# Optimization experiments

Measured on AMD Instinct MI355X. Metric: run time of the kernel, lower is better.

## Reference

```python
import jax, jax.numpy as jnp
import numpy as np

NEG_SLOPE = 0.2  # PyG GATConv default leaky_relu slope
NUM_GRAPHS = 64


def gat_layer(x, src, dst, W, a_src, a_dst, b, heads, out_ch, concat, N):
    # x: [N, in_ch] -> h: [N, H, C]
    h = (x @ W).reshape(N, heads, out_ch)
    a_s = jnp.einsum('nhc,hc->nh', h, a_src)  # [N, H]
    a_d = jnp.einsum('nhc,hc->nh', h, a_dst)  # [N, H]
    e = jax.nn.leaky_relu(a_s[src] + a_d[dst], NEG_SLOPE)  # [E, H]
    # segment softmax over edges grouped by destination node
    emax = jax.ops.segment_max(e, dst, num_segments=N)
    emax = jnp.where(jnp.isfinite(emax), emax, 0.0)
    ex = jnp.exp(e - emax[dst])
    denom = jax.ops.segment_sum(ex, dst, num_segments=N)
    alpha = ex / (denom[dst] + 1e-16)  # [E, H]
    out = jax.ops.segment_sum(alpha[:, :, None] * h[src], dst, num_segments=N)  # [N, H, C]
    out = out.reshape(N, heads * out_ch) if concat else out.mean(axis=1)
    return out + b


def setup_inputs() -> dict:
    key = jax.random.key(0)
    ks = jax.random.split(key, 16)
    N, E, F_IN, H, C, NC = 50000, 800000, 128, 4, 64, 200
    x = jax.random.normal(ks[0], (N, F_IN), dtype=jnp.float32)
    edge_index = jax.random.randint(ks[1], (2, E), 0, N, dtype=jnp.int32)
    batch = jnp.sort(jax.random.randint(ks[2], (N,), 0, NUM_GRAPHS, dtype=jnp.int32))
    s = 0.05
    params = dict(
        W1=jax.random.normal(ks[3], (F_IN, H * C), jnp.float32) * s,
        a_src1=jax.random.normal(ks[4], (H, C), jnp.float32) * s,
        a_dst1=jax.random.normal(ks[5], (H, C), jnp.float32) * s,
        b1=jnp.zeros((H * C,), jnp.float32),
        W2=jax.random.normal(ks[6], (H * C, H * C), jnp.float32) * s,
        a_src2=jax.random.normal(ks[7], (H, C), jnp.float32) * s,
        a_dst2=jax.random.normal(ks[8], (H, C), jnp.float32) * s,
        b2=jnp.zeros((H * C,), jnp.float32),
        W3=jax.random.normal(ks[9], (H * C, C), jnp.float32) * s,
        a_src3=jax.random.normal(ks[10], (1, C), jnp.float32) * s,
        a_dst3=jax.random.normal(ks[11], (1, C), jnp.float32) * s,
        b3=jnp.zeros((C,), jnp.float32),
        Wc=jax.random.normal(ks[12], (C, NC), jnp.float32) * s,
        bc=jnp.zeros((NC,), jnp.float32),
    )
    return dict(x=x, edge_index=edge_index, batch=batch, **params)


def reference(x, edge_index, batch,
              W1, a_src1, a_dst1, b1,
              W2, a_src2, a_dst2, b2,
              W3, a_src3, a_dst3, b3,
              Wc, bc):
    N = x.shape[0]
    # PyG GATConv adds self-loops by default
    loop = jnp.arange(N, dtype=edge_index.dtype)
    src = jnp.concatenate([edge_index[0], loop])
    dst = jnp.concatenate([edge_index[1], loop])
    H, C = a_src1.shape
    h = gat_layer(x, src, dst, W1, a_src1, a_dst1, b1, H, C, True, N)
    h = jax.nn.elu(h)  # dropout is identity in eval mode
    h = gat_layer(h, src, dst, W2, a_src2, a_dst2, b2, H, C, True, N)
    h = jax.nn.elu(h)
    h = gat_layer(h, src, dst, W3, a_src3, a_dst3, b3, 1, C, False, N)
    h = jax.nn.elu(h)
    # global mean pool per graph
    sums = jax.ops.segment_sum(h, batch, num_segments=NUM_GRAPHS)
    counts = jax.ops.segment_sum(jnp.ones((N,), h.dtype), batch, num_segments=NUM_GRAPHS)
    pooled = sums / jnp.maximum(counts, 1.0)[:, None]
    return pooled @ Wc + bc
```

## Files before the change

### kernel.cpp

```cpp
#include <hip/hip_runtime.h>


typedef __attribute__((ext_vector_type(8))) __bf16 bf16x8;
typedef __attribute__((ext_vector_type(4))) float f32x4;
typedef __attribute__((ext_vector_type(8))) unsigned short u16x8;

#define LOG2E 1.44269504f

static __device__ __forceinline__ unsigned short f2bf(float f) {
    unsigned u = __float_as_uint(f);
    unsigned r = (u + 0x7fffu + ((u >> 16) & 1u)) >> 16;
    return (unsigned short)r;
}
static __device__ __forceinline__ float bf2f(unsigned short s) {
    return __uint_as_float(((unsigned)s) << 16);
}

static __device__ __forceinline__ void g2lds16(const unsigned short* g,
                                               unsigned short* l) {
    __builtin_amdgcn_global_load_lds(
        (const __attribute__((address_space(1))) unsigned int*)g,
        (__attribute__((address_space(3))) unsigned int*)l, 16, 0, 0);
}

__global__ void count_edges(const int* __restrict__ ei, int* __restrict__ deg,
                            int* __restrict__ epos, int E) {
    int i = blockIdx.x * blockDim.x + threadIdx.x;
    if (i >= E) return;
    int dst = ei[E + i];
    epos[i] = atomicAdd(&deg[dst], 1);
}

__global__ __launch_bounds__(256) void scan_partial(const int* __restrict__ deg,
                                                    int* __restrict__ rowptr,
                                                    int* __restrict__ blockSums, int N) {
    int t = threadIdx.x;
    int lane = t & 63, wv = t >> 6;
    int base = blockIdx.x * 1024 + t * 4;
    int v[4];
#pragma unroll
    for (int j = 0; j < 4; ++j) v[j] = (base + j < N) ? deg[base + j] + 1 : 0;
    int local = v[0] + v[1] + v[2] + v[3];
    int x = local;
#pragma unroll
    for (int off = 1; off < 64; off <<= 1) {
        int y = __shfl_up(x, off);
        if (lane >= off) x += y;
    }
    __shared__ int wsum[4];
    if (lane == 63) wsum[wv] = x;
    __syncthreads();
    int woff = 0;
    for (int i = 0; i < wv; ++i) woff += wsum[i];
    int run = woff + x - local;
#pragma unroll
    for (int j = 0; j < 4; ++j) {
        if (base + j < N) rowptr[base + j] = run;
        run += v[j];
    }
    if (t == 255) blockSums[blockIdx.x] = woff + x;
}

__global__ void scan_blocks(int* __restrict__ blockSums, int* __restrict__ rowptr,
                            int NB, int N) {
    int lane = threadIdx.x;
    int carry = 0;
    for (int b0 = 0; b0 < NB; b0 += 64) {
        int i = b0 + lane;
        int v = (i < NB) ? blockSums[i] : 0;
        int x = v;
#pragma unroll
        for (int off = 1; off < 64; off <<= 1) {
            int y = __shfl_up(x, off);
            if (lane >= off) x += y;
        }
        if (i < NB) blockSums[i] = carry + x - v;
        carry += __shfl(x, 63);
    }
    if (lane == 0) {
        int c = N >> 10;
        int offN;
        if (c < NB) {
            offN = blockSums[c];
        } else {
            blockSums[c] = 0;
            offN = 0;
        }
        rowptr[N] = carry - offN;
    }
}

__global__ void scatter_edges(const int* __restrict__ ei, const int* __restrict__ rowptr,
                              const int* __restrict__ bs,
                              const int* __restrict__ deg, const int* __restrict__ epos,
                              int* __restrict__ srcs, int E, int N) {
    int i = blockIdx.x * blockDim.x + threadIdx.x;
    int tot = E + N;
    if (i >= tot) return;
    if (i < E) {
        int dst = ei[E + i];
        srcs[rowptr[dst] + bs[dst >> 10] + epos[i]] = ei[i];
    } else {
        int d = i - E;
        srcs[rowptr[d] + bs[d >> 10] + deg[d]] = d;
    }
}

__global__ void prep_cast(const float* __restrict__ W1, unsigned short* __restrict__ Wt1,
                          const float* __restrict__ W2, unsigned short* __restrict__ Wt2,
                          const float* __restrict__ W3, unsigned short* __restrict__ Wt3,
                          int n1, int n2, int n3, int F_IN, int HC, int C) {
    int i = blockIdx.x * blockDim.x + threadIdx.x;
    if (i < n1) {
        int n = i / F_IN, k = i - n * F_IN;
        Wt1[i] = f2bf(W1[(size_t)k * HC + n]);
        return;
    }
    i -= n1;
    if (i < n2) {
        int n = i / HC, k = i - n * HC;
        Wt2[i] = f2bf(W2[(size_t)k * HC + n]);
        return;
    }
    i -= n2;
    if (i < n3) {
        int n = i / HC, k = i - n * HC;
        Wt3[i] = f2bf(W3[(size_t)k * C + n]);
    }
}

__global__ void prep_asd(const float* __restrict__ W1, const float* __restrict__ as1,
                         const float* __restrict__ ad1,
                         const float* __restrict__ W2, const float* __restrict__ as2,
                         const float* __restrict__ ad2,
                         const float* __restrict__ W3, const float* __restrict__ as3,
                         const float* __restrict__ ad3,
                         unsigned short* __restrict__ wasd1,
                         unsigned short* __restrict__ wasd2,
                         unsigned short* __restrict__ wasd3) {
    int i = blockIdx.x * blockDim.x + threadIdx.x;
    if (i < 16 * 128) {
        int p = i >> 7, k = i & 127;
        float v = 0.f;
        if (p < 8) {
            const float* a = (p < 4) ? as1 : ad1;
            int hh = p & 3;
            for (int c = 0; c < 64; ++c)
                v += W1[(size_t)k * 256 + hh * 64 + c] * a[hh * 64 + c];
        }
        wasd1[i] = f2bf(v);
        return;
    }
    i -= 16 * 128;
    if (i < 16 * 256) {
        int p = i >> 8, k = i & 255;
        float v = 0.f;
        if (p < 8) {
            const float* a = (p < 4) ? as2 : ad2;
            int hh = p & 3;
            for (int c = 0; c < 64; ++c)
                v += W2[(size_t)k * 256 + hh * 64 + c] * a[hh * 64 + c];
        }
        wasd2[i] = f2bf(v);
        return;
    }
    i -= 16 * 256;
    if (i < 16 * 256) {
        int p = i >> 8, k = i & 255;
        float v = 0.f;
        if (p < 2) {
            const float* a = p ? ad3 : as3;
            for (int c = 0; c < 64; ++c)
                v += W3[(size_t)k * 64 + c] * a[c];
        }
        wasd3[i] = f2bf(v);
    }
}

#define BK 32

template <bool AF32, int WAVES_N>
__global__ __launch_bounds__(256) void gemm_bf16(const void* __restrict__ Av,
                                                 const unsigned short* __restrict__ Bt,
                                                 const unsigned short* __restrict__ Wasd,
                                                 unsigned short* __restrict__ C,
                                                 float* __restrict__ as_o,
                                                 float* __restrict__ ad_o,
                                                 int M, int N, int K, int H) {
    constexpr int BMt = (4 / WAVES_N) * 64;
    constexpr int BNt = WAVES_N * 64;
    constexpr int ASLOTS = BMt * 4;
    constexpr int ROUNDS = (BMt + BNt) / 64;
    constexpr bool ASD_ALL = (WAVES_N == 1);
    __shared__ unsigned short As[2][BMt * BK];
    __shared__ unsigned short Bs[2][BNt * BK];
    __shared__ unsigned short Ws[2][16 * BK];
    int t = threadIdx.x;
    int bm = blockIdx.y * BMt;
    int wave = t >> 6, lane = t & 63;
    int wm = (wave / WAVES_N) * 64, wn = (wave % WAVES_N) * 64;
    int quad = lane >> 4, mr = lane & 15;

    f32x4 zero = {0.f, 0.f, 0.f, 0.f};
    f32x4 acc[4][4];
#pragma unroll
    for (int i = 0; i < 4; ++i)
#pragma unroll
        for (int j = 0; j < 4; ++j) acc[i][j] = zero;
    f32x4 acc4[4];
#pragma unroll
    for (int i = 0; i < 4; ++i) acc4[i] = zero;

    int sw = quad ^ ((mr >> 1) & 3);
    int aoff[4], boff[4];
#pragma unroll
    for (int i = 0; i < 4; ++i) {
        aoff[i] = (wm + i * 16 + mr) * BK + sw * 8;
        boff[i] = (wn + i * 16 + mr) * BK + sw * 8;
    }

    auto stage_ab = [&](int bsel, int kk) {
        const unsigned short* Ab = (const unsigned short*)Av;
#pragma unroll
        for (int r = 0; r < ROUNDS; ++r) {
            int slotw = r * 256 + wave * 64;
            int slot = slotw + lane;
            if (slotw < ASLOTS) {
                int row = slot >> 2;
                int sg = (slot & 3) ^ ((row >> 1) & 3);
                int gra = bm + row;
                if (gra < M)
                    g2lds16(&Ab[(size_t)gra * K + kk + sg * 8], &As[bsel][slotw * 8]);
            } else {
                int bslot = slot - ASLOTS;
                int row = bslot >> 2;
                int sg = (bslot & 3) ^ ((row >> 1) & 3);
                g2lds16(&Bt[(size_t)row * K + kk + sg * 8], &Bs[bsel][(slotw - ASLOTS) * 8]);
            }
        }
        if (wave == 0)
            g2lds16(&Wasd[(size_t)(lane >> 2) * K + kk + (lane & 3) * 8], &Ws[bsel][0]);
    };
    auto stage_b_af32 = [&](int bsel, int kk) {
#pragma unroll
        for (int r = 0; r < BNt / 64; ++r) {
            int slotw = r * 256 + wave * 64;
            int bslot = slotw + lane;
            int row = bslot >> 2;
            int sg = (bslot & 3) ^ ((row >> 1) & 3);
            g2lds16(&Bt[(size_t)row * K + kk + sg * 8], &Bs[bsel][slotw * 8]);
        }
        if (wave == 0)
            g2lds16(&Wasd[(size_t)(lane >> 2) * K + kk + (lane & 3) * 8], &Ws[bsel][0]);
    };
    auto loadA_f32 = [&](int kk, float4& lo, float4& hi) {
        int slot = t, row = slot >> 2;
        int sg = (slot & 3) ^ ((row >> 1) & 3);
        int gra = bm + row;
        lo = make_float4(0.f, 0.f, 0.f, 0.f); hi = lo;
        if (gra < M) {
            const float* Af = (const float*)Av;
            lo = *(const float4*)&Af[(size_t)gra * K + kk + sg * 8];
            hi = *(const float4*)&Af[(size_t)gra * K + kk + sg * 8 + 4];
        }
    };
    auto writeA = [&](int bsel, float4 lo, float4 hi) {
        int slot = t;
        *(ushort4*)&As[bsel][slot * 8]     = make_ushort4(f2bf(lo.x), f2bf(lo.y), f2bf(lo.z), f2bf(lo.w));
        *(ushort4*)&As[bsel][slot * 8 + 4] = make_ushort4(f2bf(hi.x), f2bf(hi.y), f2bf(hi.z), f2bf(hi.w));
    };

    const int nt = K / BK;
    int cur = 0;

    if (AF32) {
        float4 l0, h0;
        loadA_f32(0, l0, h0);
        writeA(0, l0, h0);
        stage_b_af32(0, 0);
    } else {
        stage_ab(0, 0);
    }
    __syncthreads();

    for (int ts = 0; ts < nt; ++ts) {
        int nxt = cur ^ 1;
        bool more = (ts + 1 < nt);
        float4 plo, phi;
        if (more) {
            if (AF32) {
                loadA_f32((ts + 1) * BK, plo, phi);
                stage_b_af32(nxt, (ts + 1) * BK);
            } else {
                stage_ab(nxt, (ts + 1) * BK);
            }
        }
        bf16x8 af[4], bfr[4];
#pragma unroll
        for (int i = 0; i < 4; ++i) {
            af[i]  = *(bf16x8*)&As[cur][aoff[i]];
            bfr[i] = *(bf16x8*)&Bs[cur][boff[i]];
        }
#pragma unroll
        for (int i = 0; i < 4; ++i)
#pragma unroll
            for (int j = 0; j < 4; ++j)
                acc[i][j] = __builtin_amdgcn_mfma_f32_16x16x32_bf16(af[i], bfr[j], acc[i][j], 0, 0, 0);
        if (ASD_ALL || wave == 0) {
            bf16x8 wsf = *(bf16x8*)&Ws[cur][mr * BK + quad * 8];
#pragma unroll
            for (int i = 0; i < 4; ++i)
                acc4[i] = __builtin_amdgcn_mfma_f32_16x16x32_bf16(af[i], wsf, acc4[i], 0, 0, 0);
        }
        if (more && AF32) writeA(nxt, plo, phi);
        __syncthreads();
        cur = nxt;
    }

    if ((ASD_ALL || wave == 0) && mr < 2 * H) {
#pragma unroll
        for (int i = 0; i < 4; ++i)
#pragma unroll
            for (int r = 0; r < 4; ++r) {
                int grow = bm + wm + i * 16 + quad * 4 + r;
                if (grow >= M) continue;
                float v = acc4[i][r] * LOG2E;
                if (mr < H) as_o[(size_t)grow * H + mr] = v;
                else        ad_o[(size_t)grow * H + (mr - H)] = v;
            }
    }

#pragma unroll
    for (int i = 0; i < 4; ++i) {
#pragma unroll
        for (int r = 0; r < 4; ++r) {
            int grow = bm + wm + i * 16 + quad * 4 + r;
            if (grow >= M) continue;
#pragma unroll
            for (int j = 0; j < 4; ++j) {
                int gcol = wn + j * 16 + mr;
                C[(size_t)grow * N + gcol] = f2bf(acc[i][j][r]);
            }
        }
    }
}

template <int H, int NPW, int VPL, bool OUTF32>
__global__ __launch_bounds__(256) void gat_aggregate(const unsigned short* __restrict__ hbuf,
                                                     const float* __restrict__ as_i,
                                                     const float* __restrict__ ad_i,
                                                     const int* __restrict__ rowptr,
                                                     const int* __restrict__ bs,
                                                     const int* __restrict__ srcs,
                                                     const float* __restrict__ bias,
                                                     void* __restrict__ out_v, int N) {
    constexpr int LPN = 64 / NPW;
    constexpr int HC = LPN * VPL;
    int wid = (blockIdx.x * blockDim.x + threadIdx.x) >> 6;
    int lane = threadIdx.x & 63;
    int sub = lane / LPN;
    int li  = lane % LPN;
    int node = wid * NPW + sub;
    if (node >= N) return;
    int row = rowptr[node] + bs[node >> 10];
    int end = rowptr[node + 1] + bs[(node + 1) >> 10];
    int len = end - row;
    const int hd_lane = (li * VPL) >> 6;

    float advh = ad_i[(size_t)node * H + hd_lane];

    float acc[VPL];
#pragma unroll
    for (int j = 0; j < VPL; ++j) acc[j] = 0.f;
    float l = 0.f;

    const int U = 8;
    for (int base = 0; base < len; base += U) {
        int s[U];
        float cf[U];
#pragma unroll
        for (int u = 0; u < U; ++u) {
            int idx = base + u;
            int ii = row + ((idx < len) ? idx : (len - 1));
            s[u] = srcs[ii];
        }
#pragma unroll
        for (int u = 0; u < U; ++u) cf[u] = as_i[(size_t)s[u] * H + hd_lane];
        if (VPL == 8) {
            u16x8 r[U];
#pragma unroll
            for (int u = 0; u < U; ++u)
                r[u] = *(const u16x8*)&hbuf[(size_t)s[u] * HC + li * 8];
#pragma unroll
            for (int u = 0; u < U; ++u) {
                float e = cf[u] + advh;
                e = fmaxf(e, 0.2f * e);
                float wgt = (base + u < len) ? exp2f(e) : 0.f;
                l += wgt;
#pragma unroll
                for (int j = 0; j < 8; ++j) acc[j] += wgt * bf2f(r[u][j]);
            }
        } else {
            ushort4 r[U];
#pragma unroll
            for (int u = 0; u < U; ++u)
                r[u] = *(const ushort4*)&hbuf[(size_t)s[u] * HC + li * 4];
#pragma unroll
            for (int u = 0; u < U; ++u) {
                float e = cf[u] + advh;
                e = fmaxf(e, 0.2f * e);
                float wgt = (base + u < len) ? exp2f(e) : 0.f;
                l += wgt;
                acc[0] += wgt * bf2f(r[u].x);
                acc[1] += wgt * bf2f(r[u].y);
                acc[2] += wgt * bf2f(r[u].z);
                acc[3] += wgt * bf2f(r[u].w);
            }
        }
    }

    float inv_l = 1.f / (l + 1e-16f);
    float vals[VPL];
#pragma unroll
    for (int j = 0; j < VPL; ++j) {
        float v = acc[j] * inv_l + bias[li * VPL + j];
        vals[j] = (v > 0.f) ? v : (__expf(v) - 1.f);
    }
    if (OUTF32) {
        float* out = (float*)out_v;
        if (VPL == 4) {
            float4 o = make_float4(vals[0], vals[1], vals[2], vals[3]);
            *(float4*)&out[(size_t)node * HC + li * 4] = o;
        } else {
#pragma unroll
            for (int j = 0; j < VPL; ++j)
                out[(size_t)node * HC + li * VPL + j] = vals[j];
        }
    } else {
        unsigned short* out = (unsigned short*)out_v;
        if (VPL == 8) {
            u16x8 o;
#pragma unroll
            for (int j = 0; j < 8; ++j) o[j] = f2bf(vals[j]);
            *(u16x8*)&out[(size_t)node * HC + li * 8] = o;
        } else {
            ushort4 o;
            o.x = f2bf(vals[0]); o.y = f2bf(vals[1]);
            o.z = f2bf(vals[2]); o.w = f2bf(vals[3]);
            *(ushort4*)&out[(size_t)node * HC + li * 4] = o;
        }
    }
}

#define POOL_CHUNK 128
__global__ __launch_bounds__(256) void pool_kernel(const float* __restrict__ hf,
                                                   const int* __restrict__ batch,
                                                   float* __restrict__ sums,
                                                   float* __restrict__ counts, int N) {
    int t = threadIdx.x;
    int c = t & 63, sub = t >> 6;
    int start = blockIdx.x * POOL_CHUNK;
    int end = min(start + POOL_CHUNK, N);
    float acc = 0.f, cnt = 0.f;
    int cur = -1;
    for (int n = start + sub; n < end; n += 4) {
        int g = batch[n];
        if (g != cur) {
            if (cur >= 0) {
                atomicAdd(&sums[cur * 64 + c], acc);
                if (c == 0) atomicAdd(&counts[cur], cnt);
            }
            cur = g; acc = 0.f; cnt = 0.f;
        }
        acc += hf[(size_t)n * 64 + c];
        cnt += 1.f;
    }
    if (cur >= 0) {
        atomicAdd(&sums[cur * 64 + c], acc);
        if (c == 0) atomicAdd(&counts[cur], cnt);
    }
}

__global__ void classify(const float* __restrict__ sums, const float* __restrict__ counts,
                         const float* __restrict__ Wc, const float* __restrict__ bc,
                         float* __restrict__ out, int NC) {
    __shared__ float p[64];
    int g = blockIdx.x;
    if (threadIdx.x < 64) {
        float cnt = fmaxf(counts[g], 1.0f);
        p[threadIdx.x] = sums[g * 64 + threadIdx.x] / cnt;
    }
    __syncthreads();
    int k = threadIdx.x;
    if (k < NC) {
        float acc = bc[k];
        for (int c = 0; c < 64; ++c) acc += p[c] * Wc[c * NC + k];
        out[g * NC + k] = acc;
    }
}

static inline size_t align_up(size_t x, size_t a) { return (x + a - 1) / a * a; }

extern "C" void kernel_launch(void* const* d_in, const int* in_sizes, int n_in,
                              void* d_out, int out_size, void* d_ws, size_t ws_size,
                              hipStream_t stream) {
    const float* x      = (const float*)d_in[0];
    const int*   ei     = (const int*)d_in[1];
    const int*   batch  = (const int*)d_in[2];
    const float* W1     = (const float*)d_in[3];
    const float* a_src1 = (const float*)d_in[4];
    const float* a_dst1 = (const float*)d_in[5];
    const float* b1     = (const float*)d_in[6];
    const float* W2     = (const float*)d_in[7];
    const float* a_src2 = (const float*)d_in[8];
    const float* a_dst2 = (const float*)d_in[9];
    const float* b2     = (const float*)d_in[10];
    const float* W3     = (const float*)d_in[11];
    const float* a_src3 = (const float*)d_in[12];
    const float* a_dst3 = (const float*)d_in[13];
    const float* b3     = (const float*)d_in[14];
    const float* Wc     = (const float*)d_in[15];
    const float* bc     = (const float*)d_in[16];

    const int N    = in_sizes[2];
    const int E    = in_sizes[1] / 2;
    const int F_IN = in_sizes[0] / N;
    const int HC   = in_sizes[6];
    const int C    = in_sizes[14];
    const int NC   = in_sizes[16];
    const int Etot = E + N;
    const int NB   = (N + 1023) / 1024;
    const int NPB  = (N + POOL_CHUNK - 1) / POOL_CHUNK;

    char* w = (char*)d_ws;
    size_t off = 0;
    auto alloc = [&](size_t bytes) -> void* {
        void* p = w + off;
        off = align_up(off + bytes, 256);
        return p;
    };
    int*   deg    = (int*)alloc((size_t)N * 4);
    float* sums   = (float*)alloc((size_t)(64 * 64 + 64) * 4);
    float* counts = sums + 64 * 64;
    int*   rowptr = (int*)alloc((size_t)(N + 1) * 4);
    int*   epos   = (int*)alloc((size_t)E * 4);
    int*   srcs   = (int*)alloc((size_t)Etot * 4);
    int*   bsums  = (int*)alloc((size_t)(NB + 1) * 4);
    float* as_buf = (float*)alloc((size_t)N * 4 * 4);
    float* ad_buf = (float*)alloc((size_t)N * 4 * 4);
    unsigned short* Wt1 = (unsigned short*)alloc((size_t)HC * F_IN * 2);
    unsigned short* Wt2 = (unsigned short*)alloc((size_t)HC * HC * 2);
    unsigned short* Wt3 = (unsigned short*)alloc((size_t)C * HC * 2);
    unsigned short* wasd1 = (unsigned short*)alloc((size_t)16 * F_IN * 2);
    unsigned short* wasd2 = (unsigned short*)alloc((size_t)16 * HC * 2);
    unsigned short* wasd3 = (unsigned short*)alloc((size_t)16 * HC * 2);
    unsigned short* hA  = (unsigned short*)alloc((size_t)N * HC * 2);
    unsigned short* hB  = (unsigned short*)alloc((size_t)N * HC * 2);
    unsigned short* hC  = (unsigned short*)alloc((size_t)N * C * 2);
    float* bufF   = (float*)alloc((size_t)N * C * 4);

    const int TPB = 256;

    hipMemsetAsync(deg, 0, (char*)(sums + 64 * 64 + 64) - (char*)deg, stream);

    count_edges<<<(E + TPB - 1) / TPB, TPB, 0, stream>>>(ei, deg, epos, E);
    scan_partial<<<NB, 256, 0, stream>>>(deg, rowptr, bsums, N);
    scan_blocks<<<1, 64, 0, stream>>>(bsums, rowptr, NB, N);
    scatter_edges<<<(Etot + TPB - 1) / TPB, TPB, 0, stream>>>(ei, rowptr, bsums, deg, epos, srcs, E, N);

    int n1 = HC * F_IN, n2 = HC * HC, n3 = C * HC;
    int ntot = n1 + n2 + n3;
    prep_cast<<<(ntot + TPB - 1) / TPB, TPB, 0, stream>>>(
        W1, Wt1, W2, Wt2, W3, Wt3, n1, n2, n3, F_IN, HC, C);
    int nasd = 16 * F_IN + 16 * HC + 16 * HC;
    prep_asd<<<(nasd + TPB - 1) / TPB, TPB, 0, stream>>>(
        W1, a_src1, a_dst1, W2, a_src2, a_dst2, W3, a_src3, a_dst3,
        wasd1, wasd2, wasd3);

    dim3 gWide(1, (N + 63) / 64);
    dim3 gNarrow(1, (N + 255) / 256);
    int aggBlocks12 = (((N + 1) / 2) + 3) / 4;
    int aggBlocks3  = (((N + 3) / 4) + 3) / 4;

    gemm_bf16<true, 4><<<gWide, 256, 0, stream>>>(x, Wt1, wasd1, hA, as_buf, ad_buf, N, HC, F_IN, 4);
    gat_aggregate<4, 2, 8, false><<<aggBlocks12, 256, 0, stream>>>(hA, as_buf, ad_buf, rowptr, bsums, srcs, b1, hB, N);

    gemm_bf16<false, 4><<<gWide, 256, 0, stream>>>(hB, Wt2, wasd2, hA, as_buf, ad_buf, N, HC, HC, 4);
    gat_aggregate<4, 2, 8, false><<<aggBlocks12, 256, 0, stream>>>(hA, as_buf, ad_buf, rowptr, bsums, srcs, b2, hB, N);

    gemm_bf16<false, 1><<<gNarrow, 256, 0, stream>>>(hB, Wt3, wasd3, hC, as_buf, ad_buf, N, C, HC, 1);
    gat_aggregate<1, 4, 4, true><<<aggBlocks3, 256, 0, stream>>>(hC, as_buf, ad_buf, rowptr, bsums, srcs, b3, bufF, N);

    pool_kernel<<<NPB, 256, 0, stream>>>(bufF, batch, sums, counts, N);
    classify<<<64, 256, 0, stream>>>(sums, counts, Wc, bc, (float*)d_out, NC);
}
```

Baseline: 398.6 us.

## Fuse graph prep and pool/classify stages into cooperative kernels with grid sync

Replaces the memset, count, two-level scan, scatter and two weight-prep launches with a single cooperative kernel that separates phases with grid-wide barriers. The pooling and classifier kernels are merged the same way. The goal is to remove launch overhead and inter-kernel gaps for many small kernels. In exchange, a fixed 256-block grid processes the large edge loops with grid-stride loops, and grid.sync itself has a cost. The scan phase also assumes NB is no larger than the grid size (49 here).

Result: slower. 590.3 us (+48.1%).

```diff
diff --git a/kernel.cpp b/kernel.cpp
--- a/kernel.cpp
+++ b/kernel.cpp
@@ -1,4 +1,7 @@
 #include <hip/hip_runtime.h>
+#include <hip/hip_cooperative_groups.h>
+
+namespace cg = cooperative_groups;
 
 
 typedef __attribute__((ext_vector_type(8))) __bf16 bf16x8;
@@ -23,132 +26,48 @@
         (__attribute__((address_space(3))) unsigned int*)l, 16, 0, 0);
 }
 
-__global__ void count_edges(const int* __restrict__ ei, int* __restrict__ deg,
-                            int* __restrict__ epos, int E) {
-    int i = blockIdx.x * blockDim.x + threadIdx.x;
-    if (i >= E) return;
-    int dst = ei[E + i];
-    epos[i] = atomicAdd(&deg[dst], 1);
-}
-
-__global__ __launch_bounds__(256) void scan_partial(const int* __restrict__ deg,
-                                                    int* __restrict__ rowptr,
-                                                    int* __restrict__ blockSums, int N) {
-    int t = threadIdx.x;
-    int lane = t & 63, wv = t >> 6;
-    int base = blockIdx.x * 1024 + t * 4;
-    int v[4];
-#pragma unroll
-    for (int j = 0; j < 4; ++j) v[j] = (base + j < N) ? deg[base + j] + 1 : 0;
-    int local = v[0] + v[1] + v[2] + v[3];
-    int x = local;
-#pragma unroll
-    for (int off = 1; off < 64; off <<= 1) {
-        int y = __shfl_up(x, off);
-        if (lane >= off) x += y;
-    }
-    __shared__ int wsum[4];
-    if (lane == 63) wsum[wv] = x;
-    __syncthreads();
-    int woff = 0;
-    for (int i = 0; i < wv; ++i) woff += wsum[i];
-    int run = woff + x - local;
-#pragma unroll
-    for (int j = 0; j < 4; ++j) {
-        if (base + j < N) rowptr[base + j] = run;
-        run += v[j];
-    }
-    if (t == 255) blockSums[blockIdx.x] = woff + x;
-}
-
-__global__ void scan_blocks(int* __restrict__ blockSums, int* __restrict__ rowptr,
-                            int NB, int N) {
-    int lane = threadIdx.x;
-    int carry = 0;
-    for (int b0 = 0; b0 < NB; b0 += 64) {
-        int i = b0 + lane;
-        int v = (i < NB) ? blockSums[i] : 0;
-        int x = v;
-#pragma unroll
-        for (int off = 1; off < 64; off <<= 1) {
-            int y = __shfl_up(x, off);
-            if (lane >= off) x += y;
-        }
-        if (i < NB) blockSums[i] = carry + x - v;
-        carry += __shfl(x, 63);
-    }
-    if (lane == 0) {
-        int c = N >> 10;
-        int offN;
-        if (c < NB) {
-            offN = blockSums[c];
-        } else {
-            blockSums[c] = 0;
-            offN = 0;
-        }
-        rowptr[N] = carry - offN;
-    }
-}
-
-__global__ void scatter_edges(const int* __restrict__ ei, const int* __restrict__ rowptr,
-                              const int* __restrict__ bs,
-                              const int* __restrict__ deg, const int* __restrict__ epos,
-                              int* __restrict__ srcs, int E, int N) {
-    int i = blockIdx.x * blockDim.x + threadIdx.x;
-    int tot = E + N;
-    if (i >= tot) return;
-    if (i < E) {
-        int dst = ei[E + i];
-        srcs[rowptr[dst] + bs[dst >> 10] + epos[i]] = ei[i];
-    } else {
-        int d = i - E;
-        srcs[rowptr[d] + bs[d >> 10] + deg[d]] = d;
-    }
-}
-
-__global__ void prep_cast(const float* __restrict__ W1, unsigned short* __restrict__ Wt1,
-                          const float* __restrict__ W2, unsigned short* __restrict__ Wt2,
-                          const float* __restrict__ W3, unsigned short* __restrict__ Wt3,
-                          int n1, int n2, int n3, int F_IN, int HC, int C) {
-    int i = blockIdx.x * blockDim.x + threadIdx.x;
-    if (i < n1) {
-        int n = i / F_IN, k = i - n * F_IN;
-        Wt1[i] = f2bf(W1[(size_t)k * HC + n]);
+struct PrepArgs {
+    const int* ei;
+    int* deg; int* epos; int* rowptr; int* bsums; int* srcs;
+    float* zero0; int zn;
+    const float* W1; const float* W2; const float* W3;
+    const float* as1; const float* ad1;
+    const float* as2; const float* ad2;
+    const float* as3; const float* ad3;
+    unsigned short* Wt1; unsigned short* Wt2; unsigned short* Wt3;
+    unsigned short* wasd1; unsigned short* wasd2; unsigned short* wasd3;
+    int E; int N; int NB; int n1; int n2; int n3; int F_IN; int HC; int C;
+};
+
+static __device__ __forceinline__ void prep_elem(int i, const PrepArgs& a) {
+    if (i < a.n1) {
+        int n = i / a.F_IN, k = i - n * a.F_IN;
+        a.Wt1[i] = f2bf(a.W1[(size_t)k * a.HC + n]);
         return;
     }
-    i -= n1;
-    if (i < n2) {
-        int n = i / HC, k = i - n * HC;
-        Wt2[i] = f2bf(W2[(size_t)k * HC + n]);
+    i -= a.n1;
+    if (i < a.n2) {
+        int n = i / a.HC, k = i - n * a.HC;
+        a.Wt2[i] = f2bf(a.W2[(size_t)k * a.HC + n]);
         return;
     }
-    i -= n2;
-    if (i < n3) {
-        int n = i / HC, k = i - n * HC;
-        Wt3[i] = f2bf(W3[(size_t)k * C + n]);
-    }
-}
-
-__global__ void prep_asd(const float* __restrict__ W1, const float* __restrict__ as1,
-                         const float* __restrict__ ad1,
-                         const float* __restrict__ W2, const float* __restrict__ as2,
-                         const float* __restrict__ ad2,
-                         const float* __restrict__ W3, const float* __restrict__ as3,
-                         const float* __restrict__ ad3,
-                         unsigned short* __restrict__ wasd1,
-                         unsigned short* __restrict__ wasd2,
-                         unsigned short* __restrict__ wasd3) {
-    int i = blockIdx.x * blockDim.x + threadIdx.x;
+    i -= a.n2;
+    if (i < a.n3) {
+        int n = i / a.HC, k = i - n * a.HC;
+        a.Wt3[i] = f2bf(a.W3[(size_t)k * a.C + n]);
+        return;
+    }
+    i -= a.n3;
     if (i < 16 * 128) {
         int p = i >> 7, k = i & 127;
         float v = 0.f;
         if (p < 8) {
-            const float* a = (p < 4) ? as1 : ad1;
+            const float* aa = (p < 4) ? a.as1 : a.ad1;
             int hh = p & 3;
             for (int c = 0; c < 64; ++c)
-                v += W1[(size_t)k * 256 + hh * 64 + c] * a[hh * 64 + c];
-        }
-        wasd1[i] = f2bf(v);
+                v += a.W1[(size_t)k * 256 + hh * 64 + c] * aa[hh * 64 + c];
+        }
+        a.wasd1[i] = f2bf(v);
         return;
     }
     i -= 16 * 128;
@@ -156,12 +75,12 @@
         int p = i >> 8, k = i & 255;
         float v = 0.f;
         if (p < 8) {
-            const float* a = (p < 4) ? as2 : ad2;
+            const float* aa = (p < 4) ? a.as2 : a.ad2;
             int hh = p & 3;
             for (int c = 0; c < 64; ++c)
-                v += W2[(size_t)k * 256 + hh * 64 + c] * a[hh * 64 + c];
-        }
-        wasd2[i] = f2bf(v);
+                v += a.W2[(size_t)k * 256 + hh * 64 + c] * aa[hh * 64 + c];
+        }
+        a.wasd2[i] = f2bf(v);
         return;
     }
     i -= 16 * 256;
@@ -169,11 +88,100 @@
         int p = i >> 8, k = i & 255;
         float v = 0.f;
         if (p < 2) {
-            const float* a = p ? ad3 : as3;
+            const float* aa = p ? a.ad3 : a.as3;
             for (int c = 0; c < 64; ++c)
-                v += W3[(size_t)k * 64 + c] * a[c];
-        }
-        wasd3[i] = f2bf(v);
+                v += a.W3[(size_t)k * 64 + c] * aa[c];
+        }
+        a.wasd3[i] = f2bf(v);
+    }
+}
+
+__global__ __launch_bounds__(256) void fused_prep(PrepArgs a) {
+    cg::grid_group grid = cg::this_grid();
+    const int gtid = blockIdx.x * 256 + threadIdx.x;
+    const int gsz = gridDim.x * 256;
+
+    for (int i = gtid; i < a.N; i += gsz) a.deg[i] = 0;
+    for (int i = gtid; i < a.zn; i += gsz) a.zero0[i] = 0.f;
+    {
+        int ntot = a.n1 + a.n2 + a.n3 + 16 * a.F_IN + 16 * a.HC + 16 * a.HC;
+        for (int i = gtid; i < ntot; i += gsz) prep_elem(i, a);
+    }
+    grid.sync();
+
+    for (int i = gtid; i < a.E; i += gsz) {
+        int dst = a.ei[a.E + i];
+        a.epos[i] = atomicAdd(&a.deg[dst], 1);
+    }
+    grid.sync();
+
+    if (blockIdx.x < (unsigned)a.NB) {
+        int t = threadIdx.x;
+        int lane = t & 63, wv = t >> 6;
+        int base = blockIdx.x * 1024 + t * 4;
+        int v[4];
+#pragma unroll
+        for (int j = 0; j < 4; ++j) v[j] = (base + j < a.N) ? a.deg[base + j] + 1 : 0;
+        int local = v[0] + v[1] + v[2] + v[3];
+        int x = local;
+#pragma unroll
+        for (int off = 1; off < 64; off <<= 1) {
+            int y = __shfl_up(x, off);
+            if (lane >= off) x += y;
+        }
+        __shared__ int wsum[4];
+        if (lane == 63) wsum[wv] = x;
+        __syncthreads();
+        int woff = 0;
+        for (int i = 0; i < wv; ++i) woff += wsum[i];
+        int run = woff + x - local;
+#pragma unroll
+        for (int j = 0; j < 4; ++j) {
+            if (base + j < a.N) a.rowptr[base + j] = run;
+            run += v[j];
+        }
+        if (t == 255) a.bsums[blockIdx.x] = woff + x;
+    }
+    grid.sync();
+
+    if (blockIdx.x == 0 && threadIdx.x < 64) {
+        int lane = threadIdx.x;
+        int carry = 0;
+        for (int b0 = 0; b0 < a.NB; b0 += 64) {
+            int i = b0 + lane;
+            int v = (i < a.NB) ? a.bsums[i] : 0;
+            int x = v;
+#pragma unroll
+            for (int off = 1; off < 64; off <<= 1) {
+                int y = __shfl_up(x, off);
+                if (lane >= off) x += y;
+            }
+            if (i < a.NB) a.bsums[i] = carry + x - v;
+            carry += __shfl(x, 63);
+        }
+        if (lane == 0) {
+            int c = a.N >> 10;
+            int offN;
+            if (c < a.NB) {
+                offN = a.bsums[c];
+            } else {
+                a.bsums[c] = 0;
+                offN = 0;
+            }
+            a.rowptr[a.N] = carry - offN;
+        }
+    }
+    grid.sync();
+
+    int tot = a.E + a.N;
+    for (int i = gtid; i < tot; i += gsz) {
+        if (i < a.E) {
+            int dst = a.ei[a.E + i];
+            a.srcs[a.rowptr[dst] + a.bsums[dst >> 10] + a.epos[i]] = a.ei[i];
+        } else {
+            int d = i - a.E;
+            a.srcs[a.rowptr[d] + a.bsums[d >> 10] + a.deg[d]] = d;
+        }
     }
 }
 
@@ -453,49 +461,56 @@
 }
 
 #define POOL_CHUNK 128
-__global__ __launch_bounds__(256) void pool_kernel(const float* __restrict__ hf,
-                                                   const int* __restrict__ batch,
-                                                   float* __restrict__ sums,
-                                                   float* __restrict__ counts, int N) {
+struct PoolArgs {
+    const float* hf; const int* batch;
+    float* sums; float* counts;
+    const float* Wc; const float* bc; float* out;
+    int N; int NC; int NPB;
+};
+
+__global__ __launch_bounds__(256) void pool_classify(PoolArgs a) {
+    cg::grid_group grid = cg::this_grid();
     int t = threadIdx.x;
     int c = t & 63, sub = t >> 6;
-    int start = blockIdx.x * POOL_CHUNK;
-    int end = min(start + POOL_CHUNK, N);
-    float acc = 0.f, cnt = 0.f;
-    int cur = -1;
-    for (int n = start + sub; n < end; n += 4) {
-        int g = batch[n];
-        if (g != cur) {
-            if (cur >= 0) {
-                atomicAdd(&sums[cur * 64 + c], acc);
-                if (c == 0) atomicAdd(&counts[cur], cnt);
-            }
-            cur = g; acc = 0.f; cnt = 0.f;
-        }
-        acc += hf[(size_t)n * 64 + c];
-        cnt += 1.f;
-    }
-    if (cur >= 0) {
-        atomicAdd(&sums[cur * 64 + c], acc);
-        if (c == 0) atomicAdd(&counts[cur], cnt);
-    }
-}
-
-__global__ void classify(const float* __restrict__ sums, const float* __restrict__ counts,
-                         const float* __restrict__ Wc, const float* __restrict__ bc,
-                         float* __restrict__ out, int NC) {
-    __shared__ float p[64];
-    int g = blockIdx.x;
-    if (threadIdx.x < 64) {
-        float cnt = fmaxf(counts[g], 1.0f);
-        p[threadIdx.x] = sums[g * 64 + threadIdx.x] / cnt;
-    }
-    __syncthreads();
-    int k = threadIdx.x;
-    if (k < NC) {
-        float acc = bc[k];
-        for (int c = 0; c < 64; ++c) acc += p[c] * Wc[c * NC + k];
-        out[g * NC + k] = acc;
+
+    for (int cb = blockIdx.x; cb < a.NPB; cb += gridDim.x) {
+        int start = cb * POOL_CHUNK;
+        int end = min(start + POOL_CHUNK, a.N);
+        float acc = 0.f, cnt = 0.f;
+        int cur = -1;
+        for (int n = start + sub; n < end; n += 4) {
+            int g = a.batch[n];
+            if (g != cur) {
+                if (cur >= 0) {
+                    atomicAdd(&a.sums[cur * 64 + c], acc);
+                    if (c == 0) atomicAdd(&a.counts[cur], cnt);
+                }
+                cur = g; acc = 0.f; cnt = 0.f;
+            }
+            acc += a.hf[(size_t)n * 64 + c];
+            cnt += 1.f;
+        }
+        if (cur >= 0) {
+            atomicAdd(&a.sums[cur * 64 + c], acc);
+            if (c == 0) atomicAdd(&a.counts[cur], cnt);
+        }
+    }
+    grid.sync();
+
+    if (blockIdx.x < 64) {
+        __shared__ float p[64];
+        int g = blockIdx.x;
+        if (t < 64) {
+            float cnt = fmaxf(a.counts[g], 1.0f);
+            p[t] = a.sums[g * 64 + t] / cnt;
+        }
+        __syncthreads();
+        int k = t;
+        if (k < a.NC) {
+            float acc = a.bc[k];
+            for (int cc = 0; cc < 64; ++cc) acc += p[cc] * a.Wc[cc * a.NC + k];
+            a.out[g * a.NC + k] = acc;
+        }
     }
 }
 
@@ -528,9 +543,9 @@
     const int HC   = in_sizes[6];
     const int C    = in_sizes[14];
     const int NC   = in_sizes[16];
-    const int Etot = E + N;
     const int NB   = (N + 1023) / 1024;
     const int NPB  = (N + POOL_CHUNK - 1) / POOL_CHUNK;
+    const int Etot = E + N;
 
     char* w = (char*)d_ws;
     size_t off = 0;
@@ -559,23 +574,24 @@
     unsigned short* hC  = (unsigned short*)alloc((size_t)N * C * 2);
     float* bufF   = (float*)alloc((size_t)N * C * 4);
 
-    const int TPB = 256;
-
-    hipMemsetAsync(deg, 0, (char*)(sums + 64 * 64 + 64) - (char*)deg, stream);
-
-    count_edges<<<(E + TPB - 1) / TPB, TPB, 0, stream>>>(ei, deg, epos, E);
-    scan_partial<<<NB, 256, 0, stream>>>(deg, rowptr, bsums, N);
-    scan_blocks<<<1, 64, 0, stream>>>(bsums, rowptr, NB, N);
-    scatter_edges<<<(Etot + TPB - 1) / TPB, TPB, 0, stream>>>(ei, rowptr, bsums, deg, epos, srcs, E, N);
-
-    int n1 = HC * F_IN, n2 = HC * HC, n3 = C * HC;
-    int ntot = n1 + n2 + n3;
-    prep_cast<<<(ntot + TPB - 1) / TPB, TPB, 0, stream>>>(
-        W1, Wt1, W2, Wt2, W3, Wt3, n1, n2, n3, F_IN, HC, C);
-    int nasd = 16 * F_IN + 16 * HC + 16 * HC;
-    prep_asd<<<(nasd + TPB - 1) / TPB, TPB, 0, stream>>>(
-        W1, a_src1, a_dst1, W2, a_src2, a_dst2, W3, a_src3, a_dst3,
-        wasd1, wasd2, wasd3);
+    PrepArgs pa;
+    pa.ei = ei; pa.deg = deg; pa.epos = epos; pa.rowptr = rowptr;
+    pa.bsums = bsums; pa.srcs = srcs;
+    pa.zero0 = sums; pa.zn = 64 * 64 + 64;
+    pa.W1 = W1; pa.W2 = W2; pa.W3 = W3;
+    pa.as1 = a_src1; pa.ad1 = a_dst1;
+    pa.as2 = a_src2; pa.ad2 = a_dst2;
+    pa.as3 = a_src3; pa.ad3 = a_dst3;
+    pa.Wt1 = Wt1; pa.Wt2 = Wt2; pa.Wt3 = Wt3;
+    pa.wasd1 = wasd1; pa.wasd2 = wasd2; pa.wasd3 = wasd3;
+    pa.E = E; pa.N = N; pa.NB = NB;
+    pa.n1 = HC * F_IN; pa.n2 = HC * HC; pa.n3 = C * HC;
+    pa.F_IN = F_IN; pa.HC = HC; pa.C = C;
+    {
+        void* args[] = {&pa};
+        hipLaunchCooperativeKernel((void*)fused_prep, dim3(256), dim3(256),
+                                   args, 0, stream);
+    }
 
     dim3 gWide(1, (N + 63) / 64);
     dim3 gNarrow(1, (N + 255) / 256);
@@ -591,6 +607,13 @@
     gemm_bf16<false, 1><<<gNarrow, 256, 0, stream>>>(hB, Wt3, wasd3, hC, as_buf, ad_buf, N, C, HC, 1);
     gat_aggregate<1, 4, 4, true><<<aggBlocks3, 256, 0, stream>>>(hC, as_buf, ad_buf, rowptr, bsums, srcs, b3, bufF, N);
 
-    pool_kernel<<<NPB, 256, 0, stream>>>(bufF, batch, sums, counts, N);
-    classify<<<64, 256, 0, stream>>>(sums, counts, Wc, bc, (float*)d_out, NC);
-}
+    PoolArgs qa;
+    qa.hf = bufF; qa.batch = batch; qa.sums = sums; qa.counts = counts;
+    qa.Wc = Wc; qa.bc = bc; qa.out = (float*)d_out;
+    qa.N = N; qa.NC = NC; qa.NPB = NPB;
+    {
+        void* args[] = {&qa};
+        hipLaunchCooperativeKernel((void*)pool_classify, dim3(256), dim3(256),
+                                   args, 0, stream);
+    }
+}
```

## Store layer 1-2 node features as FP8 to halve gather traffic

Applied to the files above, without the earlier changes.

The first two GEMMs now write their projected node features in FP8 E4M3 instead of bf16, and the matching aggregation kernels read 8 bytes per lane and unpack them with packed FP8-to-float conversions. The goal is to halve the bytes moved by the random edge gathers, which dominate aggregation cost, and also to halve the GEMM output writes. The two weight-prep kernels are merged into one launch to save a launch. The cost is lower precision for intermediate features (about 3 mantissa bits, no scaling), which may hurt accuracy.

Result: faster. 343.5 us (-13.8%).

```diff
diff --git a/kernel.cpp b/kernel.cpp
--- a/kernel.cpp
+++ b/kernel.cpp
@@ -1,8 +1,10 @@
 #include <hip/hip_runtime.h>
+#include <hip/hip_fp8.h>
 
 
 typedef __attribute__((ext_vector_type(8))) __bf16 bf16x8;
 typedef __attribute__((ext_vector_type(4))) float f32x4;
+typedef __attribute__((ext_vector_type(2))) float f32x2;
 typedef __attribute__((ext_vector_type(8))) unsigned short u16x8;
 
 #define LOG2E 1.44269504f
@@ -15,6 +17,35 @@
 static __device__ __forceinline__ float bf2f(unsigned short s) {
     return __uint_as_float(((unsigned)s) << 16);
 }
+
+#if __has_builtin(__builtin_amdgcn_cvt_pk_fp8_f32)
+static __device__ __forceinline__ unsigned char f2fp8(float v) {
+    return (unsigned char)(__builtin_amdgcn_cvt_pk_fp8_f32(v, v, 0, false) & 0xff);
+}
+#else
+static __device__ __forceinline__ unsigned char f2fp8(float v) {
+    return (unsigned char)__hip_cvt_float_to_fp8(v, __HIP_SATFINITE, __HIP_E4M3);
+}
+#endif
+
+#if __has_builtin(__builtin_amdgcn_cvt_pk_f32_fp8)
+template <bool HI>
+static __device__ __forceinline__ void fp8pair(unsigned int w, float& a, float& b) {
+    f32x2 r = __builtin_amdgcn_cvt_pk_f32_fp8(w, HI);
+    a = r[0]; b = r[1];
+}
+#else
+static __device__ __forceinline__ float fp8one(unsigned char x) {
+    __half_raw hr = __hip_cvt_fp8_to_halfraw((__hip_fp8_storage_t)x, __HIP_E4M3);
+    return __half2float(*(const __half*)&hr);
+}
+template <bool HI>
+static __device__ __forceinline__ void fp8pair(unsigned int w, float& a, float& b) {
+    unsigned int s = HI ? (w >> 16) : w;
+    a = fp8one((unsigned char)(s & 0xff));
+    b = fp8one((unsigned char)((s >> 8) & 0xff));
+}
+#endif
 
 static __device__ __forceinline__ void g2lds16(const unsigned short* g,
                                                unsigned short* l) {
@@ -106,10 +137,16 @@
     }
 }
 
-__global__ void prep_cast(const float* __restrict__ W1, unsigned short* __restrict__ Wt1,
-                          const float* __restrict__ W2, unsigned short* __restrict__ Wt2,
-                          const float* __restrict__ W3, unsigned short* __restrict__ Wt3,
-                          int n1, int n2, int n3, int F_IN, int HC, int C) {
+__global__ void prep_weights(const float* __restrict__ W1, unsigned short* __restrict__ Wt1,
+                             const float* __restrict__ W2, unsigned short* __restrict__ Wt2,
+                             const float* __restrict__ W3, unsigned short* __restrict__ Wt3,
+                             const float* __restrict__ as1, const float* __restrict__ ad1,
+                             const float* __restrict__ as2, const float* __restrict__ ad2,
+                             const float* __restrict__ as3, const float* __restrict__ ad3,
+                             unsigned short* __restrict__ wasd1,
+                             unsigned short* __restrict__ wasd2,
+                             unsigned short* __restrict__ wasd3,
+                             int n1, int n2, int n3, int F_IN, int HC, int C) {
     int i = blockIdx.x * blockDim.x + threadIdx.x;
     if (i < n1) {
         int n = i / F_IN, k = i - n * F_IN;
@@ -126,19 +163,9 @@
     if (i < n3) {
         int n = i / HC, k = i - n * HC;
         Wt3[i] = f2bf(W3[(size_t)k * C + n]);
-    }
-}
-
-__global__ void prep_asd(const float* __restrict__ W1, const float* __restrict__ as1,
-                         const float* __restrict__ ad1,
-                         const float* __restrict__ W2, const float* __restrict__ as2,
-                         const float* __restrict__ ad2,
-                         const float* __restrict__ W3, const float* __restrict__ as3,
-                         const float* __restrict__ ad3,
-                         unsigned short* __restrict__ wasd1,
-                         unsigned short* __restrict__ wasd2,
-                         unsigned short* __restrict__ wasd3) {
-    int i = blockIdx.x * blockDim.x + threadIdx.x;
+        return;
+    }
+    i -= n3;
     if (i < 16 * 128) {
         int p = i >> 7, k = i & 127;
         float v = 0.f;
@@ -179,11 +206,11 @@
 
 #define BK 32
 
-template <bool AF32, int WAVES_N>
+template <bool AF32, int WAVES_N, bool C8>
 __global__ __launch_bounds__(256) void gemm_bf16(const void* __restrict__ Av,
                                                  const unsigned short* __restrict__ Bt,
                                                  const unsigned short* __restrict__ Wasd,
-                                                 unsigned short* __restrict__ C,
+                                                 void* __restrict__ Cv,
                                                  float* __restrict__ as_o,
                                                  float* __restrict__ ad_o,
                                                  int M, int N, int K, int H) {
@@ -339,14 +366,18 @@
 #pragma unroll
             for (int j = 0; j < 4; ++j) {
                 int gcol = wn + j * 16 + mr;
-                C[(size_t)grow * N + gcol] = f2bf(acc[i][j][r]);
-            }
-        }
-    }
-}
-
-template <int H, int NPW, int VPL, bool OUTF32>
-__global__ __launch_bounds__(256) void gat_aggregate(const unsigned short* __restrict__ hbuf,
+                if constexpr (C8) {
+                    ((unsigned char*)Cv)[(size_t)grow * N + gcol] = f2fp8(acc[i][j][r]);
+                } else {
+                    ((unsigned short*)Cv)[(size_t)grow * N + gcol] = f2bf(acc[i][j][r]);
+                }
+            }
+        }
+    }
+}
+
+template <int H, int NPW, int VPL, bool OUTF32, bool IN8>
+__global__ __launch_bounds__(256) void gat_aggregate(const void* __restrict__ hbuf_v,
                                                      const float* __restrict__ as_i,
                                                      const float* __restrict__ ad_i,
                                                      const int* __restrict__ rowptr,
@@ -386,25 +417,45 @@
         }
 #pragma unroll
         for (int u = 0; u < U; ++u) cf[u] = as_i[(size_t)s[u] * H + hd_lane];
-        if (VPL == 8) {
-            u16x8 r[U];
+        if constexpr (IN8 && VPL == 8) {
+            const unsigned char* hb = (const unsigned char*)hbuf_v;
+            uint2 r[U];
 #pragma unroll
             for (int u = 0; u < U; ++u)
-                r[u] = *(const u16x8*)&hbuf[(size_t)s[u] * HC + li * 8];
+                r[u] = *(const uint2*)&hb[(size_t)s[u] * HC + li * VPL];
 #pragma unroll
             for (int u = 0; u < U; ++u) {
                 float e = cf[u] + advh;
                 e = fmaxf(e, 0.2f * e);
                 float wgt = (base + u < len) ? exp2f(e) : 0.f;
                 l += wgt;
+                float v0, v1;
+                fp8pair<false>(r[u].x, v0, v1); acc[0] += wgt * v0; acc[1] += wgt * v1;
+                fp8pair<true>(r[u].x, v0, v1);  acc[2] += wgt * v0; acc[3] += wgt * v1;
+                fp8pair<false>(r[u].y, v0, v1); acc[4] += wgt * v0; acc[5] += wgt * v1;
+                fp8pair<true>(r[u].y, v0, v1);  acc[6] += wgt * v0; acc[7] += wgt * v1;
+            }
+        } else if constexpr (VPL == 8) {
+            const unsigned short* hb = (const unsigned short*)hbuf_v;
+            u16x8 r[U];
+#pragma unroll
+            for (int u = 0; u < U; ++u)
+                r[u] = *(const u16x8*)&hb[(size_t)s[u] * HC + li * 8];
+#pragma unroll
+            for (int u = 0; u < U; ++u) {
+                float e = cf[u] + advh;
+                e = fmaxf(e, 0.2f * e);
+                float wgt = (base + u < len) ? exp2f(e) : 0.f;
+                l += wgt;
 #pragma unroll
                 for (int j = 0; j < 8; ++j) acc[j] += wgt * bf2f(r[u][j]);
             }
         } else {
+            const unsigned short* hb = (const unsigned short*)hbuf_v;
             ushort4 r[U];
 #pragma unroll
             for (int u = 0; u < U; ++u)
-                r[u] = *(const ushort4*)&hbuf[(size_t)s[u] * HC + li * 4];
+                r[u] = *(const ushort4*)&hb[(size_t)s[u] * HC + li * 4];
 #pragma unroll
             for (int u = 0; u < U; ++u) {
                 float e = cf[u] + advh;
@@ -426,9 +477,9 @@
         float v = acc[j] * inv_l + bias[li * VPL + j];
         vals[j] = (v > 0.f) ? v : (__expf(v) - 1.f);
     }
-    if (OUTF32) {
+    if constexpr (OUTF32) {
         float* out = (float*)out_v;
-        if (VPL == 4) {
+        if constexpr (VPL == 4) {
             float4 o = make_float4(vals[0], vals[1], vals[2], vals[3]);
             *(float4*)&out[(size_t)node * HC + li * 4] = o;
         } else {
@@ -438,7 +489,7 @@
         }
     } else {
         unsigned short* out = (unsigned short*)out_v;
-        if (VPL == 8) {
+        if constexpr (VPL == 8) {
             u16x8 o;
 #pragma unroll
             for (int j = 0; j < 8; ++j) o[j] = f2bf(vals[j]);
@@ -554,14 +605,14 @@
     unsigned short* wasd1 = (unsigned short*)alloc((size_t)16 * F_IN * 2);
     unsigned short* wasd2 = (unsigned short*)alloc((size_t)16 * HC * 2);
     unsigned short* wasd3 = (unsigned short*)alloc((size_t)16 * HC * 2);
-    unsigned short* hA  = (unsigned short*)alloc((size_t)N * HC * 2);
+    unsigned char*  hA  = (unsigned char*)alloc((size_t)N * HC);
     unsigned short* hB  = (unsigned short*)alloc((size_t)N * HC * 2);
     unsigned short* hC  = (unsigned short*)alloc((size_t)N * C * 2);
     float* bufF   = (float*)alloc((size_t)N * C * 4);
 
     const int TPB = 256;
 
-    hipMemsetAsync(deg, 0, (char*)(sums + 64 * 64 + 64) - (char*)deg, stream);
+    (void)hipMemsetAsync(deg, 0, (char*)(sums + 64 * 64 + 64) - (char*)deg, stream);
 
     count_edges<<<(E + TPB - 1) / TPB, TPB, 0, stream>>>(ei, deg, epos, E);
     scan_partial<<<NB, 256, 0, stream>>>(deg, rowptr, bsums, N);
@@ -569,27 +620,25 @@
     scatter_edges<<<(Etot + TPB - 1) / TPB, TPB, 0, stream>>>(ei, rowptr, bsums, deg, epos, srcs, E, N);
 
     int n1 = HC * F_IN, n2 = HC * HC, n3 = C * HC;
-    int ntot = n1 + n2 + n3;
-    prep_cast<<<(ntot + TPB - 1) / TPB, TPB, 0, stream>>>(
-        W1, Wt1, W2, Wt2, W3, Wt3, n1, n2, n3, F_IN, HC, C);
-    int nasd = 16 * F_IN + 16 * HC + 16 * HC;
-    prep_asd<<<(nasd + TPB - 1) / TPB, TPB, 0, stream>>>(
-        W1, a_src1, a_dst1, W2, a_src2, a_dst2, W3, a_src3, a_dst3,
-        wasd1, wasd2, wasd3);
+    int ntot = n1 + n2 + n3 + 16 * F_IN + 16 * HC + 16 * HC;
+    prep_weights<<<(ntot + TPB - 1) / TPB, TPB, 0, stream>>>(
+        W1, Wt1, W2, Wt2, W3, Wt3,
+        a_src1, a_dst1, a_src2, a_dst2, a_src3, a_dst3,
+        wasd1, wasd2, wasd3, n1, n2, n3, F_IN, HC, C);
 
     dim3 gWide(1, (N + 63) / 64);
     dim3 gNarrow(1, (N + 255) / 256);
     int aggBlocks12 = (((N + 1) / 2) + 3) / 4;
     int aggBlocks3  = (((N + 3) / 4) + 3) / 4;
 
-    gemm_bf16<true, 4><<<gWide, 256, 0, stream>>>(x, Wt1, wasd1, hA, as_buf, ad_buf, N, HC, F_IN, 4);
-    gat_aggregate<4, 2, 8, false><<<aggBlocks12, 256, 0, stream>>>(hA, as_buf, ad_buf, rowptr, bsums, srcs, b1, hB, N);
-
-    gemm_bf16<false, 4><<<gWide, 256, 0, stream>>>(hB, Wt2, wasd2, hA, as_buf, ad_buf, N, HC, HC, 4);
-    gat_aggregate<4, 2, 8, false><<<aggBlocks12, 256, 0, stream>>>(hA, as_buf, ad_buf, rowptr, bsums, srcs, b2, hB, N);
-
-    gemm_bf16<false, 1><<<gNarrow, 256, 0, stream>>>(hB, Wt3, wasd3, hC, as_buf, ad_buf, N, C, HC, 1);
-    gat_aggregate<1, 4, 4, true><<<aggBlocks3, 256, 0, stream>>>(hC, as_buf, ad_buf, rowptr, bsums, srcs, b3, bufF, N);
+    gemm_bf16<true, 4, true><<<gWide, 256, 0, stream>>>(x, Wt1, wasd1, hA, as_buf, ad_buf, N, HC, F_IN, 4);
+    gat_aggregate<4, 2, 8, false, true><<<aggBlocks12, 256, 0, stream>>>(hA, as_buf, ad_buf, rowptr, bsums, srcs, b1, hB, N);
+
+    gemm_bf16<false, 4, true><<<gWide, 256, 0, stream>>>(hB, Wt2, wasd2, hA, as_buf, ad_buf, N, HC, HC, 4);
+    gat_aggregate<4, 2, 8, false, true><<<aggBlocks12, 256, 0, stream>>>(hA, as_buf, ad_buf, rowptr, bsums, srcs, b2, hB, N);
+
+    gemm_bf16<false, 1, false><<<gNarrow, 256, 0, stream>>>(hB, Wt3, wasd3, hC, as_buf, ad_buf, N, C, HC, 1);
+    gat_aggregate<1, 4, 4, true, false><<<aggBlocks3, 256, 0, stream>>>(hC, as_buf, ad_buf, rowptr, bsums, srcs, b3, bufF, N);
 
     pool_kernel<<<NPB, 256, 0, stream>>>(bufF, batch, sums, counts, N);
     classify<<<64, 256, 0, stream>>>(sums, counts, Wc, bc, (float*)d_out, NC);
```
